# Kernel tuning notes

Hardware: AMD Instinct MI355X
Metric: run time of the kernel (lower is better)

## Reference

```python
import jax, jax.numpy as jnp
import numpy as np

N_DATA = 12288
N_QUERY = 12288
DIM = 3
RADIUS = 0.085  # gives ~32 neighbors/query for uniform points in [0,1]^3


def setup_inputs() -> dict:
    key = jax.random.key(0)
    k1, k2 = jax.random.split(key)
    data = jax.random.uniform(k1, (N_DATA, DIM), dtype=jnp.float32)
    queries = jax.random.uniform(k2, (N_QUERY, DIM), dtype=jnp.float32)
    radius = jnp.float32(RADIUS)
    return {"data": data, "queries": queries, "radius": radius}


def reference(data, queries, radius):
    # Dense, jit-compatible equivalent of KDTree.query_radius with return_distance=True.
    # Original returns ragged CSR (neighbors_index, neighbors_row_splits, weights=dists**2).
    # Fixed-shape encoding: boolean membership mask [M, N] (row m, col n True iff
    # data[n] is a neighbor of queries[m]; CSR indices = nonzero cols in row order),
    # row_splits [M+1] (exact CSR splits), and dense weights [M, N] = squared
    # distance where within radius else 0 (CSR weights = masked entries in row order).
    sq_d = jnp.sum(data * data, axis=-1)          # [N]
    sq_q = jnp.sum(queries * queries, axis=-1)    # [M]
    # ||q - d||^2 = ||q||^2 + ||d||^2 - 2 q.d  (GEMM form)
    d2 = sq_q[:, None] + sq_d[None, :] - 2.0 * (queries @ data.T)  # [M, N]
    d2 = jnp.maximum(d2, 0.0)
    mask = d2 <= radius * radius                  # [M, N]
    counts = jnp.sum(mask, axis=-1, dtype=jnp.int32)  # [M]
    row_splits = jnp.concatenate(
        [jnp.zeros((1,), jnp.int32), jnp.cumsum(counts)]
    )  # [M+1], matches nbr_dict['neighbors_row_splits']
    weights = jnp.where(mask, d2, 0.0)            # dists**2, masked
    return row_splits, mask, weights
```

## Files before the change

### kernel.cpp

```cpp
#include <hip/hip_runtime.h>


__global__ __launch_bounds__(256) void nbr_kernel(
    const float* __restrict__ data,
    const float* __restrict__ queries,
    const float* __restrict__ radius_p,
    float* __restrict__ out,
    int* __restrict__ counts,
    int N, long long mask_off, long long w_off)
{
    const int m = blockIdx.x;
    const int tid = threadIdx.x;

    const float r = radius_p[0];
    const float r2 = __fmul_rn(r, r);
    const float q0 = queries[3 * m + 0];
    const float q1 = queries[3 * m + 1];
    const float q2 = queries[3 * m + 2];
    const float sq_q = __fadd_rn(
        __fadd_rn(__fmul_rn(q0, q0), __fmul_rn(q1, q1)), __fmul_rn(q2, q2));

    float* mask_row = out + mask_off + (long long)m * N;
    float* w_row    = out + w_off    + (long long)m * N;

    int cnt = 0;

    auto compute = [&](int n, float& mv, float& wv) -> int {
        const float d0 = data[3 * n + 0];
        const float d1 = data[3 * n + 1];
        const float d2e = data[3 * n + 2];
        const float sq_d = __fadd_rn(
            __fadd_rn(__fmul_rn(d0, d0), __fmul_rn(d1, d1)), __fmul_rn(d2e, d2e));
        const float dot = __fmaf_rn(q2, d2e, __fmaf_rn(q1, d1, __fmul_rn(q0, d0)));
        const float s = __fadd_rn(sq_q, sq_d);
        float v = __fsub_rn(s, __fmul_rn(2.0f, dot));
        v = fmaxf(v, 0.0f);
        const bool in = (v <= r2);
        mv = in ? 1.0f : 0.0f;
        wv = in ? v : 0.0f;
        return in ? 1 : 0;
    };

    if (tid < 3) {
        float mv, wv;
        cnt += compute(tid, mv, wv);
        mask_row[tid] = mv;
        w_row[tid] = wv;
    } else if (tid == 3) {
        float mv, wv;
        cnt += compute(N - 1, mv, wv);
        mask_row[N - 1] = mv;
        w_row[N - 1] = wv;
    }

    const int nchunks = (N - 4) >> 2;
    for (int j = tid; j < nchunks; j += 256) {
        const int n = 3 + 4 * j;
        float4 mv4, wv4;
        cnt += compute(n + 0, mv4.x, wv4.x);
        cnt += compute(n + 1, mv4.y, wv4.y);
        cnt += compute(n + 2, mv4.z, wv4.z);
        cnt += compute(n + 3, mv4.w, wv4.w);
        *reinterpret_cast<float4*>(mask_row + n) = mv4;
        *reinterpret_cast<float4*>(w_row + n) = wv4;
    }

    for (int off = 32; off > 0; off >>= 1) cnt += __shfl_down(cnt, off);
    __shared__ int lds_cnt;
    if (tid == 0) lds_cnt = 0;
    __syncthreads();
    if ((tid & 63) == 0) atomicAdd(&lds_cnt, cnt);
    __syncthreads();
    if (tid == 0) counts[m] = lds_cnt;
}

__global__ __launch_bounds__(256) void scan_kernel(
    const int* __restrict__ counts, float* __restrict__ out, int M)
{
    __shared__ int sums[256];
    const int t = threadIdx.x;
    const int CH = (M + 255) / 256;
    const int base = t * CH;

    int local[64];
    int s = 0;
    for (int i = 0; i < CH; ++i) {
        const int v = (base + i < M) ? counts[base + i] : 0;
        local[i] = v;
        s += v;
    }
    sums[t] = s;
    __syncthreads();
    for (int off = 1; off < 256; off <<= 1) {
        const int v = (t >= off) ? sums[t - off] : 0;
        __syncthreads();
        sums[t] += v;
        __syncthreads();
    }
    int prefix = sums[t] - s;
    for (int i = 0; i < CH; ++i) {
        if (base + i < M) out[base + i] = (float)prefix;
        prefix += local[i];
    }
    if (t == 255) out[M] = (float)prefix;
}

extern "C" void kernel_launch(void* const* d_in, const int* in_sizes, int n_in,
                              void* d_out, int out_size, void* d_ws, size_t ws_size,
                              hipStream_t stream) {
    const float* data    = (const float*)d_in[0];
    const float* queries = (const float*)d_in[1];
    const float* radius  = (const float*)d_in[2];

    const int N = in_sizes[0] / 3;
    const int M = in_sizes[1] / 3;

    float* out = (float*)d_out;
    int* counts = (int*)d_ws;

    const long long mask_off = (long long)M + 1;
    const long long w_off = mask_off + (long long)M * N;

    nbr_kernel<<<M, 256, 0, stream>>>(data, queries, radius, out, counts,
                                      N, mask_off, w_off);
    scan_kernel<<<1, 256, 0, stream>>>(counts, out, M);
}
```

Measured before the change: 1.263 ms.

## Precompute packed query/data norms and sweep flat output with grid-stride kernel

Adds a pre-pass that packs each point and query into a float4 holding xyz plus its squared norm. A persistent grid-stride kernel then walks the whole flattened M×N output in aligned float4 chunks, which lets the vector stores line up with the odd output offset and removes per-row block scheduling. Per-row counts are accumulated with global atomics instead of a block reduction. The fast path is specialised to a compile-time N=12288, which adds extra launches and atomic contention while cutting redundant norm recomputation and the strided 3-float loads.

```diff
diff --git a/kernel.cpp b/kernel.cpp
--- a/kernel.cpp
+++ b/kernel.cpp
@@ -1,7 +1,98 @@
 #include <hip/hip_runtime.h>
 
 
-__global__ __launch_bounds__(256) void nbr_kernel(
+#define GRID_MAIN 2048
+
+__global__ __launch_bounds__(256) void pre_kernel(
+    const float* __restrict__ data, const float* __restrict__ queries,
+    int M, int N, int* __restrict__ counts,
+    float4* __restrict__ qpre, float4* __restrict__ dpre)
+{
+    const int t = blockIdx.x * 256 + threadIdx.x;
+    if (t < M) {
+        const float q0 = queries[3 * t], q1 = queries[3 * t + 1], q2 = queries[3 * t + 2];
+        const float sq = __fadd_rn(
+            __fadd_rn(__fmul_rn(q0, q0), __fmul_rn(q1, q1)), __fmul_rn(q2, q2));
+        qpre[t] = make_float4(q0, q1, q2, sq);
+        counts[t] = 0;
+    }
+    if (t < N) {
+        const float d0 = data[3 * t], d1 = data[3 * t + 1], d2 = data[3 * t + 2];
+        const float sq = __fadd_rn(
+            __fadd_rn(__fmul_rn(d0, d0), __fmul_rn(d1, d1)), __fmul_rn(d2, d2));
+        dpre[t] = make_float4(d0, d1, d2, sq);
+    }
+}
+
+template <int N>
+__global__ __launch_bounds__(256) void sweep_kernel(
+    const float* __restrict__ radius_p, float* __restrict__ out,
+    int* __restrict__ counts,
+    const float4* __restrict__ qpre, const float4* __restrict__ dpre,
+    int M, long long mask_off, long long w_off)
+{
+    const float r = radius_p[0];
+    const float r2 = __fmul_rn(r, r);
+    const long long F = (long long)M * N;
+    const int K = (int)((F - 4) >> 2);
+
+    auto comp = [&](const float4& q, const float4& d, float& mve, float& wve) -> int {
+        const float dot = __fmaf_rn(q.z, d.z, __fmaf_rn(q.y, d.y, __fmul_rn(q.x, d.x)));
+        float v = __fmaf_rn(-2.0f, dot, __fadd_rn(q.w, d.w));
+        v = fmaxf(v, 0.0f);
+        const bool in = (v <= r2);
+        mve = in ? 1.0f : 0.0f;
+        wve = in ? v : 0.0f;
+        return in ? 1 : 0;
+    };
+
+    if (blockIdx.x == 0 && threadIdx.x < 4) {
+        const long long f = (threadIdx.x < 3) ? (long long)threadIdx.x : (F - 1);
+        const int m = (int)(f / N);
+        const int n = (int)(f - (long long)m * N);
+        float mv, wv;
+        const int c = comp(qpre[m], dpre[n], mv, wv);
+        out[mask_off + f] = mv;
+        out[w_off + f] = wv;
+        if (c) atomicAdd(&counts[m], 1);
+    }
+
+    const int stride = gridDim.x * 256;
+    for (int k = blockIdx.x * 256 + threadIdx.x; k < K; k += stride) {
+        const int f0 = 3 + 4 * k;
+        const int m = f0 / N;
+        const int n0 = f0 - m * N;
+        float4 mv, wv;
+        if (n0 <= N - 4) {
+            const float4 q = qpre[m];
+            const float4 da = dpre[n0 + 0];
+            const float4 db = dpre[n0 + 1];
+            const float4 dc = dpre[n0 + 2];
+            const float4 dd = dpre[n0 + 3];
+            int c = comp(q, da, mv.x, wv.x);
+            c += comp(q, db, mv.y, wv.y);
+            c += comp(q, dc, mv.z, wv.z);
+            c += comp(q, dd, mv.w, wv.w);
+            if (c) atomicAdd(&counts[m], c);
+        } else {
+            #pragma unroll
+            for (int e = 0; e < 4; ++e) {
+                const int fe = f0 + e;
+                const int me = fe / N;
+                const int ne = fe - me * N;
+                float mve, wve;
+                const int c = comp(qpre[me], dpre[ne], mve, wve);
+                reinterpret_cast<float*>(&mv)[e] = mve;
+                reinterpret_cast<float*>(&wv)[e] = wve;
+                if (c) atomicAdd(&counts[me], 1);
+            }
+        }
+        *reinterpret_cast<float4*>(out + mask_off + f0) = mv;
+        *reinterpret_cast<float4*>(out + w_off + f0) = wv;
+    }
+}
+
+__global__ __launch_bounds__(256) void nbr_kernel_generic(
     const float* __restrict__ data,
     const float* __restrict__ queries,
     const float* __restrict__ radius_p,
@@ -11,60 +102,26 @@
 {
     const int m = blockIdx.x;
     const int tid = threadIdx.x;
-
     const float r = radius_p[0];
     const float r2 = __fmul_rn(r, r);
-    const float q0 = queries[3 * m + 0];
-    const float q1 = queries[3 * m + 1];
-    const float q2 = queries[3 * m + 2];
+    const float q0 = queries[3 * m], q1 = queries[3 * m + 1], q2 = queries[3 * m + 2];
     const float sq_q = __fadd_rn(
         __fadd_rn(__fmul_rn(q0, q0), __fmul_rn(q1, q1)), __fmul_rn(q2, q2));
-
     float* mask_row = out + mask_off + (long long)m * N;
     float* w_row    = out + w_off    + (long long)m * N;
-
     int cnt = 0;
-
-    auto compute = [&](int n, float& mv, float& wv) -> int {
-        const float d0 = data[3 * n + 0];
-        const float d1 = data[3 * n + 1];
-        const float d2e = data[3 * n + 2];
+    for (int n = tid; n < N; n += 256) {
+        const float d0 = data[3 * n], d1 = data[3 * n + 1], d2e = data[3 * n + 2];
         const float sq_d = __fadd_rn(
             __fadd_rn(__fmul_rn(d0, d0), __fmul_rn(d1, d1)), __fmul_rn(d2e, d2e));
         const float dot = __fmaf_rn(q2, d2e, __fmaf_rn(q1, d1, __fmul_rn(q0, d0)));
-        const float s = __fadd_rn(sq_q, sq_d);
-        float v = __fsub_rn(s, __fmul_rn(2.0f, dot));
+        float v = __fmaf_rn(-2.0f, dot, __fadd_rn(sq_q, sq_d));
         v = fmaxf(v, 0.0f);
         const bool in = (v <= r2);
-        mv = in ? 1.0f : 0.0f;
-        wv = in ? v : 0.0f;
-        return in ? 1 : 0;
-    };
-
-    if (tid < 3) {
-        float mv, wv;
-        cnt += compute(tid, mv, wv);
-        mask_row[tid] = mv;
-        w_row[tid] = wv;
-    } else if (tid == 3) {
-        float mv, wv;
-        cnt += compute(N - 1, mv, wv);
-        mask_row[N - 1] = mv;
-        w_row[N - 1] = wv;
+        mask_row[n] = in ? 1.0f : 0.0f;
+        w_row[n] = in ? v : 0.0f;
+        cnt += in ? 1 : 0;
     }
-
-    const int nchunks = (N - 4) >> 2;
-    for (int j = tid; j < nchunks; j += 256) {
-        const int n = 3 + 4 * j;
-        float4 mv4, wv4;
-        cnt += compute(n + 0, mv4.x, wv4.x);
-        cnt += compute(n + 1, mv4.y, wv4.y);
-        cnt += compute(n + 2, mv4.z, wv4.z);
-        cnt += compute(n + 3, mv4.w, wv4.w);
-        *reinterpret_cast<float4*>(mask_row + n) = mv4;
-        *reinterpret_cast<float4*>(w_row + n) = wv4;
-    }
-
     for (int off = 32; off > 0; off >>= 1) cnt += __shfl_down(cnt, off);
     __shared__ int lds_cnt;
     if (tid == 0) lds_cnt = 0;
@@ -116,12 +173,25 @@
     const int M = in_sizes[1] / 3;
 
     float* out = (float*)d_out;
+
     int* counts = (int*)d_ws;
+    const size_t cnt_bytes = ((size_t)M * sizeof(int) + 15) & ~(size_t)15;
+    float4* qpre = (float4*)((char*)d_ws + cnt_bytes);
+    float4* dpre = qpre + M;
 
     const long long mask_off = (long long)M + 1;
     const long long w_off = mask_off + (long long)M * N;
 
-    nbr_kernel<<<M, 256, 0, stream>>>(data, queries, radius, out, counts,
-                                      N, mask_off, w_off);
+    const size_t ws_need = cnt_bytes + (size_t)(M + N) * sizeof(float4);
+    if (N == 12288 && M == 12288 && ws_size >= ws_need) {
+        const int pre_blocks = (max(M, N) + 255) / 256;
+        pre_kernel<<<pre_blocks, 256, 0, stream>>>(data, queries, M, N,
+                                                   counts, qpre, dpre);
+        sweep_kernel<12288><<<GRID_MAIN, 256, 0, stream>>>(
+            radius, out, counts, qpre, dpre, M, mask_off, w_off);
+    } else {
+        nbr_kernel_generic<<<M, 256, 0, stream>>>(data, queries, radius, out,
+                                                  counts, N, mask_off, w_off);
+    }
     scan_kernel<<<1, 256, 0, stream>>>(counts, out, M);
 }
```

Result: slower. 1.385 ms (+9.7%).
